# Kernel tuning notes

Measured on AMD Instinct MI355X. Metric: run time of the kernel, lower is better.

## Reference

```python
import jax, jax.numpy as jnp
import numpy as np

DIM = 1024
N_HEADS = 16
HEAD_DIM = DIM // N_HEADS
SCALE = HEAD_DIM ** -0.5


def setup_inputs() -> dict:
    key = jax.random.key(0)
    kx, kq, kk, kv = jax.random.split(key, 4)
    x = jax.random.normal(kx, (2, 2048, DIM), dtype=jnp.float32)
    bv_q = jax.random.normal(kq, (N_HEADS, HEAD_DIM), dtype=jnp.float32) * 0.02
    bv_k = jax.random.normal(kk, (N_HEADS, HEAD_DIM), dtype=jnp.float32) * 0.02
    bv_v = jax.random.normal(kv, (N_HEADS, HEAD_DIM), dtype=jnp.float32) * 0.02
    return {"x": x, "bv_q": bv_q, "bv_k": bv_k, "bv_v": bv_v}


def reference(x, bv_q, bv_k, bv_v):
    B, T, D = x.shape
    H, HD = N_HEADS, HEAD_DIM
    x_h = x.reshape(B, T, H, HD)
    # sign-gated Q/K/V (sign of binding vectors; elementwise +/-1 gating)
    Q = x_h * jnp.sign(bv_q)  # [B,T,H,HD]
    K = x_h * jnp.sign(bv_k)
    V = x_h * jnp.sign(bv_v)
    # causal scores, sigmoid gating (no softmax)
    scores = jnp.einsum('bqhd,bkhd->bhqk', Q, K) * SCALE  # [B,H,T,T]
    causal = jnp.tril(jnp.ones((T, T), dtype=bool))
    attn = jnp.where(causal, jax.nn.sigmoid(scores * 4.0), 0.0)
    out = jnp.einsum('bhqk,bkhd->bqhd', attn, V)  # [B,T,H,HD]
    return out.reshape(B, T, D)
```

## Files before the change

kernel.cpp:

```cpp
#include <hip/hip_runtime.h>
#include <hip/hip_bf16.h>
#include <stdint.h>

#define DIM 1024
#define T_LEN 2048
#define NB 2
#define NH 16
#define HD 64
#define NQT 32

typedef float f32x2 __attribute__((ext_vector_type(2)));
typedef float f32x4 __attribute__((ext_vector_type(4)));
typedef float f32x16 __attribute__((ext_vector_type(16)));
typedef __bf16 bf16x8 __attribute__((ext_vector_type(8)));
typedef __bf16 bf16x2 __attribute__((ext_vector_type(2)));
typedef unsigned int u32;
typedef unsigned int u32x4 __attribute__((ext_vector_type(4)));

#define TK(qt, lo, cnt, dst) ((u32)((qt) | ((lo) << 6) | ((cnt) << 12) | ((dst) << 18)))
__constant__ u32 TASKS[80] = {
    TK(31,0,16,1), TK(31,16,16,2), TK(30,15,16,2), TK(15,0,16,0),
    TK(30,0,15,1), TK(29,0,15,1),  TK(29,15,15,2), TK(28,14,15,2), TK(14,0,15,0),
    TK(28,0,14,1), TK(27,0,14,1),  TK(27,14,14,2), TK(26,13,14,2), TK(13,0,14,0),
    TK(26,0,13,1), TK(25,0,13,1),  TK(25,13,13,2), TK(24,12,13,2), TK(12,0,13,0),
    TK(24,0,12,1), TK(23,0,12,1),  TK(23,12,12,2), TK(22,11,12,2), TK(11,0,12,0),
    TK(22,0,11,1), TK(21,0,11,1),  TK(21,11,11,2), TK(20,10,11,2), TK(10,0,11,0),
    TK(20,0,10,1), TK(19,0,10,1),  TK(19,10,10,2), TK(18,9,10,2),  TK(9,0,10,0),
    TK(18,0,9,1),  TK(17,0,9,1),   TK(17,9,9,2),   TK(16,8,9,2),   TK(8,0,9,0),
    TK(16,0,8,1),  TK(7,0,8,0),
    TK(6,0,7,0), TK(5,0,6,0), TK(4,0,5,0), TK(3,0,4,0),
    TK(2,0,3,0), TK(1,0,2,0), TK(0,0,1,0),
    TK(31,0,32,0), TK(30,0,31,0), TK(29,0,30,0), TK(28,0,29,0),
    TK(27,0,28,0), TK(26,0,27,0), TK(25,0,26,0), TK(24,0,25,0),
    TK(23,0,24,0), TK(22,0,23,0), TK(21,0,22,0), TK(20,0,21,0),
    TK(19,0,20,0), TK(18,0,19,0), TK(17,0,18,0), TK(16,0,17,0),
    TK(15,0,16,0), TK(14,0,15,0), TK(13,0,14,0), TK(12,0,13,0),
    TK(11,0,12,0), TK(10,0,11,0), TK(9,0,10,0),  TK(8,0,9,0),
    TK(7,0,8,0),   TK(6,0,7,0),   TK(5,0,6,0),   TK(4,0,5,0),
    TK(3,0,4,0),   TK(2,0,3,0),   TK(1,0,2,0),   TK(0,0,1,0),
};
#define NSPLIT 48

__device__ __forceinline__ float sgnf(float v) {
    return (v > 0.f) ? 1.f : ((v < 0.f) ? -1.f : 0.f);
}

__device__ __forceinline__ float sigmoid_half(float v) {
    return __builtin_amdgcn_rcpf(1.f + __builtin_amdgcn_exp2f(-0.72134752f * v));
}

__device__ __forceinline__ u32 pack2(float p0, float p1) {
    bf16x2 t = {(__bf16)p0, (__bf16)p1};
    return __builtin_bit_cast(u32, t);
}

__device__ __forceinline__ void gload16(const __bf16* g, __bf16* l) {
    __builtin_amdgcn_global_load_lds(
        (__attribute__((address_space(1))) void*)g,
        (__attribute__((address_space(3))) void*)l,
        16, 0, 0);
}

__global__ __launch_bounds__(256) void prep_kernel(
    const float* __restrict__ x, const float* __restrict__ bvv,
    __bf16* __restrict__ xb, __bf16* __restrict__ xt)
{
    __shared__ __align__(16) __bf16 tile[64][72];

    const int bid = blockIdx.x;
    const int h = bid & 15, tmp = bid >> 4, tt = tmp & 31, b = tmp >> 5;
    const int tid = threadIdx.x;
    const int r = tid >> 2, c0 = (tid & 3) * 16;

    const size_t rowbase = ((size_t)(b * T_LEN + tt * 64 + r)) * DIM + h * HD + c0;
    const float* xp = x + rowbase;

    __bf16 v[16];
    #pragma unroll
    for (int i = 0; i < 16; i += 4) {
        f32x4 f = *(const f32x4*)(xp + i);
        #pragma unroll
        for (int j = 0; j < 4; ++j) v[i + j] = (__bf16)f[j];
    }
    bf16x8 s0, s1;
    #pragma unroll
    for (int j = 0; j < 8; ++j) { s0[j] = v[j]; s1[j] = v[8 + j]; }
    *(bf16x8*)(xb + rowbase)     = s0;
    *(bf16x8*)(xb + rowbase + 8) = s1;
    *(bf16x8*)&tile[r][c0]     = s0;
    *(bf16x8*)&tile[r][c0 + 8] = s1;

    __syncthreads();

    const int d = tid >> 2, t0c = (tid & 3) * 16;
    const float g = sgnf(bvv[h * HD + d]);
    __bf16 ov[16];
    #pragma unroll
    for (int i = 0; i < 16; ++i) ov[i] = (__bf16)((float)tile[t0c + i][d] * g);
    bf16x8 o0, o1;
    #pragma unroll
    for (int j = 0; j < 8; ++j) { o0[j] = ov[j]; o1[j] = ov[8 + j]; }
    const size_t obase = ((size_t)((b * NH + h) * HD + d)) * T_LEN + tt * 64 + t0c;
    *(bf16x8*)(xt + obase)     = o0;
    *(bf16x8*)(xt + obase + 8) = o1;
}

__global__ __launch_bounds__(256, 4) void mba_main(
    const __bf16* __restrict__ xb, const __bf16* __restrict__ xt,
    const float* __restrict__ bvq, const float* __restrict__ bvk,
    float* __restrict__ out, float* __restrict__ ws2, int tbase)
{
    __shared__ __align__(16) __bf16 Kb[3][64][64];
    __shared__ __align__(16) __bf16 Vb[2][64][64];

    const int bid = blockIdx.x;
    const u32 tk = TASKS[tbase + (bid >> 5)];
    const int qt  = tk & 63;
    const int lo  = (tk >> 6) & 63;
    const int CL  = (tk >> 12) & 63;
    const int dst = tk >> 18;

    const int bh = bid & 31;
    const int b = bh >> 4, h = bh & 15;
    const int q0 = qt * 64;

    const int tid = threadIdx.x;
    const int w = tid >> 6, l = tid & 63;
    const int c = l & 31, hi = l >> 5;
    const int qh = w & 1, sh = w >> 1;

    const size_t xb_bh = (size_t)b * T_LEN * DIM + h * HD;
    const size_t xt_bh = (size_t)((b * NH + h) * HD) * T_LEN;

    const int rr = l >> 3;
    const int sw = ((l & 7) ^ rr) << 3;

    auto STAGE_K = [&](int buf, int kvt) {
        const int kv0s = kvt * 64;
        #pragma unroll
        for (int pt = 0; pt < 2; ++pt) {
            const int r0 = w * 8 + pt * 32;
            gload16(xb + xb_bh + (size_t)(kv0s + r0 + rr) * DIM + sw, &Kb[buf][r0][0]);
        }
    };
    auto STAGE_V = [&](int buf, int kvt) {
        const int kv0s = kvt * 64;
        #pragma unroll
        for (int pt = 0; pt < 2; ++pt) {
            const int r0 = w * 8 + pt * 32;
            gload16(xt + xt_bh + (size_t)(r0 + rr) * T_LEN + kv0s + sw, &Vb[buf][r0][0]);
        }
    };

    STAGE_K(0, lo);
    STAGE_V(0, lo);
    if (CL >= 2) STAGE_K(1, lo + 1);

    bf16x8 qa[4];
    {
        const float* bq = bvq + h * HD;
        const float* bk = bvk + h * HD;
        const int qrow = q0 + qh * 32 + c;
        #pragma unroll
        for (int m = 0; m < 4; ++m) {
            const int d0 = m * 16 + hi * 8;
            bf16x8 va = *(const bf16x8*)(xb + xb_bh + (size_t)qrow * DIM + d0);
            #pragma unroll
            for (int j = 0; j < 8; ++j) {
                float f = sgnf(bq[d0 + j]) * sgnf(bk[d0 + j]);
                qa[m][j] = (__bf16)((float)va[j] * f);
            }
        }
    }

    f32x16 o[2];
    #pragma unroll
    for (int nd = 0; nd < 2; ++nd)
        #pragma unroll
        for (int i = 0; i < 16; ++i) o[nd][i] = 0.f;

    int cur = 0;
    const int krow = sh * 32 + c;
    const int swz = (c & 7) << 4;

    for (int lt = 0; lt < CL; ++lt) {
        const int gt = lo + lt;
        const bool last_local = (lt == CL - 1);
        const bool diag = (gt == qt);
        if (last_local) { asm volatile("s_waitcnt vmcnt(0)" ::: "memory"); }
        else            { asm volatile("s_waitcnt vmcnt(2)" ::: "memory"); }
        __builtin_amdgcn_sched_barrier(0);
        __builtin_amdgcn_s_barrier();
        __builtin_amdgcn_sched_barrier(0);

        if (lt + 1 < CL) STAGE_V((lt + 1) & 1, gt + 1);
        __builtin_amdgcn_sched_barrier(0);
        if (lt + 2 < CL) {
            int stg = cur + 2; if (stg >= 3) stg -= 3;
            STAGE_K(stg, gt + 2);
        }
        __builtin_amdgcn_sched_barrier(0);

        f32x16 ss;
        #pragma unroll
        for (int i = 0; i < 16; ++i) ss[i] = 0.f;
        #pragma unroll
        for (int m = 0; m < 4; ++m) {
            bf16x8 kf = *(const bf16x8*)((const char*)&Kb[cur][krow][0]
                          + ((m * 32 + hi * 16) ^ swz));
            ss = __builtin_amdgcn_mfma_f32_32x32x16_bf16(kf, qa[m], ss, 0, 0, 0);
        }

        u32 W[8];
        #pragma unroll
        for (int i = 0; i < 8; ++i) {
            const int r0 = 2 * i;
            const int sl = (r0 & 3) + 8 * (r0 >> 2) + 4 * hi;
            float p0 = sigmoid_half(ss[r0]);
            float p1 = sigmoid_half(ss[r0 + 1]);
            if (diag) {
                const int sg = sh * 32 + sl;
                const int qg = qh * 32 + c;
                if (sg > qg)     p0 = 0.f;
                if (sg + 1 > qg) p1 = 0.f;
            }
            W[i] = pack2(p0, p1);
        }

        asm volatile("v_permlane32_swap_b32 %0, %1" : "+v"(W[0]), "+v"(W[2]));
        asm volatile("v_permlane32_swap_b32 %0, %1" : "+v"(W[1]), "+v"(W[3]));
        asm volatile("v_permlane32_swap_b32 %0, %1" : "+v"(W[4]), "+v"(W[6]));
        asm volatile("v_permlane32_swap_b32 %0, %1" : "+v"(W[5]), "+v"(W[7]));
        bf16x8 pa[2];
        pa[0] = __builtin_bit_cast(bf16x8, (u32x4){W[0], W[1], W[2], W[3]});
        pa[1] = __builtin_bit_cast(bf16x8, (u32x4){W[4], W[5], W[6], W[7]});

        #pragma unroll
        for (int m = 0; m < 2; ++m) {
            #pragma unroll
            for (int nd = 0; nd < 2; ++nd) {
                bf16x8 vf = *(const bf16x8*)((const char*)&Vb[lt & 1][nd * 32 + c][0]
                              + ((sh * 64 + m * 32 + hi * 16) ^ swz));
                o[nd] = __builtin_amdgcn_mfma_f32_32x32x16_bf16(pa[m], vf, o[nd], 0, 0, 0);
            }
        }
        cur = (cur == 2) ? 0 : cur + 1;
    }

    __syncthreads();
    float (*osc)[64] = (float(*)[64]) & Kb[0][0][0];

    if (sh == 1) {
        #pragma unroll
        for (int r = 0; r < 16; ++r) {
            const int qloc = (r & 3) + 8 * (r >> 2) + 4 * hi;
            osc[qh * 32 + qloc][c]      = o[0][r];
            osc[qh * 32 + qloc][32 + c] = o[1][r];
        }
    }
    __syncthreads();
    if (sh == 0) {
        if (dst == 0) {
            #pragma unroll
            for (int r = 0; r < 16; ++r) {
                const int qloc = (r & 3) + 8 * (r >> 2) + 4 * hi;
                const size_t row = (size_t)(b * T_LEN + q0 + qh * 32 + qloc) * DIM + h * HD;
                out[row + c]      = o[0][r] + osc[qh * 32 + qloc][c];
                out[row + 32 + c] = o[1][r] + osc[qh * 32 + qloc][32 + c];
            }
        } else {
            float* wp = ws2 + (size_t)((((qt - 16) * 32 + bh) * 2) + (dst - 1)) * 4096;
            #pragma unroll
            for (int r = 0; r < 16; ++r) {
                const int qloc = (r & 3) + 8 * (r >> 2) + 4 * hi;
                const int qrow = qh * 32 + qloc;
                wp[qrow * 64 + c]      = o[0][r] + osc[qrow][c];
                wp[qrow * 64 + 32 + c] = o[1][r] + osc[qrow][32 + c];
            }
        }
    }
}

__global__ __launch_bounds__(256) void reduce_kernel(
    const float* __restrict__ ws2, float* __restrict__ out)
{
    const int bid = blockIdx.x;
    const int tile = bid >> 2, q4 = bid & 3;
    const int qtw = tile >> 5, bh = tile & 31;
    const int b = bh >> 4, h = bh & 15;

    const float* pa = ws2 + (size_t)((qtw * 32 + bh) * 2) * 4096;
    const float* pb = pa + 4096;

    const int e = q4 * 1024 + threadIdx.x * 4;
    const int qr = e >> 6, d = e & 63;

    f32x4 va = *(const f32x4*)(pa + e);
    f32x4 vb = *(const f32x4*)(pb + e);
    f32x4 s = va + vb;
    *(f32x4*)(out + (size_t)(b * T_LEN + (16 + qtw) * 64 + qr) * DIM + h * HD + d) = s;
}

__global__ __launch_bounds__(256) void mba_fallback(
    const float* __restrict__ x,
    const float* __restrict__ bvq,
    const float* __restrict__ bvk,
    const float* __restrict__ bvv,
    float* __restrict__ out)
{
    __shared__ __align__(16) __bf16 Kb[64][72];
    __shared__ __align__(16) __bf16 Vt[HD][72];
    __shared__ __align__(16) __bf16 Pb[4][16][72];

    const int bid = blockIdx.x;
    const int qt  = (NQT - 1) - (bid & (NQT - 1));
    const int bh  = bid >> 5;
    const int b   = bh >> 4;
    const int h   = bh & 15;

    const int tid = threadIdx.x;
    const int w   = tid >> 6;
    const int l   = tid & 63;
    const int lq  = l & 15;
    const int lh  = l >> 4;

    const int  q0    = qt * 64;
    const long xbase = ((long)b * T_LEN) * DIM + h * HD;

    bf16x8 qa[2];
    {
        const int   qrow = q0 + w * 16 + lq;
        const float* qp  = x + xbase + (long)qrow * DIM + lh * 8;
        const float* gp  = bvq + h * HD + lh * 8;
        #pragma unroll
        for (int ks = 0; ks < 2; ++ks)
            #pragma unroll
            for (int j = 0; j < 8; ++j)
                qa[ks][j] = (__bf16)(qp[ks * 32 + j] * sgnf(gp[ks * 32 + j]));
    }

    f32x4 o[4];
    #pragma unroll
    for (int n = 0; n < 4; ++n) o[n] = (f32x4){0.f, 0.f, 0.f, 0.f};

    const int r_st = tid >> 2;
    const int c0   = (tid & 3) * 16;
    const float* gk = bvk + h * HD + c0;
    const float* gv = bvv + h * HD + c0;

    for (int kvt = 0; kvt <= qt; ++kvt) {
        const int kv0 = kvt * 64;
        __syncthreads();
        {
            const float* kp = x + xbase + (long)(kv0 + r_st) * DIM + c0;
            __bf16 kb[16];
            #pragma unroll
            for (int i = 0; i < 16; ++i) kb[i] = (__bf16)(kp[i] * sgnf(gk[i]));
            *(bf16x8*)&Kb[r_st][c0]     = *(bf16x8*)&kb[0];
            *(bf16x8*)&Kb[r_st][c0 + 8] = *(bf16x8*)&kb[8];
            #pragma unroll
            for (int i = 0; i < 16; ++i)
                Vt[c0 + i][r_st] = (__bf16)(kp[i] * sgnf(gv[i]));
        }
        __syncthreads();

        f32x4 s[4];
        #pragma unroll
        for (int n = 0; n < 4; ++n) s[n] = (f32x4){0.f, 0.f, 0.f, 0.f};
        #pragma unroll
        for (int ks = 0; ks < 2; ++ks)
            #pragma unroll
            for (int n = 0; n < 4; ++n) {
                bf16x8 kf = *(const bf16x8*)&Kb[n * 16 + lq][ks * 32 + lh * 8];
                s[n] = __builtin_amdgcn_mfma_f32_16x16x32_bf16(qa[ks], kf, s[n], 0, 0, 0);
            }

        const bool diag = (kvt == qt);
        #pragma unroll
        for (int n = 0; n < 4; ++n)
            #pragma unroll
            for (int j = 0; j < 4; ++j) {
                float sc = s[n][j];
                float p = __builtin_amdgcn_rcpf(
                              1.f + __builtin_amdgcn_exp2f(-0.72134752f * sc));
                if (diag && (n * 16 + lq) > (w * 16 + lh * 4 + j)) p = 0.f;
                Pb[w][lh * 4 + j][n * 16 + lq] = (__bf16)p;
            }

        #pragma unroll
        for (int ks = 0; ks < 2; ++ks) {
            bf16x8 pf = *(const bf16x8*)&Pb[w][lq][ks * 32 + lh * 8];
            #pragma unroll
            for (int n = 0; n < 4; ++n) {
                bf16x8 vf = *(const bf16x8*)&Vt[n * 16 + lq][ks * 32 + lh * 8];
                o[n] = __builtin_amdgcn_mfma_f32_16x16x32_bf16(pf, vf, o[n], 0, 0, 0);
            }
        }
    }

    float* op = out + ((long)b * T_LEN + q0 + w * 16) * DIM + h * HD;
    #pragma unroll
    for (int n = 0; n < 4; ++n)
        #pragma unroll
        for (int j = 0; j < 4; ++j)
            op[(long)(lh * 4 + j) * DIM + n * 16 + lq] = o[n][j];
}

extern "C" void kernel_launch(void* const* d_in, const int* in_sizes, int n_in,
                              void* d_out, int out_size, void* d_ws, size_t ws_size,
                              hipStream_t stream) {
    (void)in_sizes; (void)n_in; (void)out_size;
    const float* x   = (const float*)d_in[0];
    const float* bvq = (const float*)d_in[1];
    const float* bvk = (const float*)d_in[2];
    const float* bvv = (const float*)d_in[3];
    float* out = (float*)d_out;

    const size_t XB_BYTES = (size_t)NB * T_LEN * DIM * sizeof(__bf16);
    const size_t XT_BYTES = XB_BYTES;
    const size_t W2_BYTES = (size_t)16 * 32 * 2 * 4096 * sizeof(float);

    if (ws_size < XB_BYTES + XT_BYTES) {
        mba_fallback<<<NB * NH * NQT, 256, 0, stream>>>(x, bvq, bvk, bvv, out);
        return;
    }

    __bf16* xb = (__bf16*)d_ws;
    __bf16* xt = xb + (size_t)NB * T_LEN * DIM;

    prep_kernel<<<NB * NQT * NH, 256, 0, stream>>>(x, bvv, xb, xt);

    if (ws_size >= XB_BYTES + XT_BYTES + W2_BYTES) {
        float* ws2 = (float*)((char*)d_ws + XB_BYTES + XT_BYTES);
        mba_main<<<NSPLIT * 32, 256, 0, stream>>>(xb, xt, bvq, bvk, out, ws2, 0);
        reduce_kernel<<<2048, 256, 0, stream>>>(ws2, out);
    } else {
        mba_main<<<32 * 32, 256, 0, stream>>>(xb, xt, bvq, bvk, out, nullptr, 48);
    }
}
```

Before: 53.63 us.

## Precompute gated Q in prep, unroll KV loop by six with static buffer indices

The prep kernel now also writes a Q tensor pre-multiplied by sign(bq)*sign(bk), so the main kernel loads Q fragments directly instead of recomputing the gating per element. The main loop is unrolled by six with compile-time K (triple) and V (double) buffer indices, and the staging addresses advance through pointer increments. The sigmoid uses a packed multiply/add form and a v_cvt_pk_bf16_f32 instruction. The cost is an extra 8MB workspace write and read, plus larger code.

```diff
diff --git a/kernel.cpp b/kernel.cpp
--- a/kernel.cpp
+++ b/kernel.cpp
@@ -16,6 +16,8 @@
 typedef __bf16 bf16x2 __attribute__((ext_vector_type(2)));
 typedef unsigned int u32;
 typedef unsigned int u32x4 __attribute__((ext_vector_type(4)));
+
+template <int N> struct ICT { static constexpr int v = N; };
 
 #define TK(qt, lo, cnt, dst) ((u32)((qt) | ((lo) << 6) | ((cnt) << 12) | ((dst) << 18)))
 __constant__ u32 TASKS[80] = {
@@ -45,15 +47,6 @@
     return (v > 0.f) ? 1.f : ((v < 0.f) ? -1.f : 0.f);
 }
 
-__device__ __forceinline__ float sigmoid_half(float v) {
-    return __builtin_amdgcn_rcpf(1.f + __builtin_amdgcn_exp2f(-0.72134752f * v));
-}
-
-__device__ __forceinline__ u32 pack2(float p0, float p1) {
-    bf16x2 t = {(__bf16)p0, (__bf16)p1};
-    return __builtin_bit_cast(u32, t);
-}
-
 __device__ __forceinline__ void gload16(const __bf16* g, __bf16* l) {
     __builtin_amdgcn_global_load_lds(
         (__attribute__((address_space(1))) void*)g,
@@ -62,8 +55,9 @@
 }
 
 __global__ __launch_bounds__(256) void prep_kernel(
-    const float* __restrict__ x, const float* __restrict__ bvv,
-    __bf16* __restrict__ xb, __bf16* __restrict__ xt)
+    const float* __restrict__ x, const float* __restrict__ bvq,
+    const float* __restrict__ bvk, const float* __restrict__ bvv,
+    __bf16* __restrict__ xb, __bf16* __restrict__ xq, __bf16* __restrict__ xt)
 {
     __shared__ __align__(16) __bf16 tile[64][72];
 
@@ -75,18 +69,27 @@
     const size_t rowbase = ((size_t)(b * T_LEN + tt * 64 + r)) * DIM + h * HD + c0;
     const float* xp = x + rowbase;
 
-    __bf16 v[16];
+    float f[16];
     #pragma unroll
     for (int i = 0; i < 16; i += 4) {
-        f32x4 f = *(const f32x4*)(xp + i);
-        #pragma unroll
-        for (int j = 0; j < 4; ++j) v[i + j] = (__bf16)f[j];
-    }
-    bf16x8 s0, s1;
-    #pragma unroll
-    for (int j = 0; j < 8; ++j) { s0[j] = v[j]; s1[j] = v[8 + j]; }
+        f32x4 v4 = *(const f32x4*)(xp + i);
+        #pragma unroll
+        for (int j = 0; j < 4; ++j) f[i + j] = v4[j];
+    }
+    bf16x8 s0, s1, g0, g1;
+    #pragma unroll
+    for (int j = 0; j < 8; ++j) {
+        s0[j] = (__bf16)f[j];
+        s1[j] = (__bf16)f[8 + j];
+        float gq0 = sgnf(bvq[h * HD + c0 + j])     * sgnf(bvk[h * HD + c0 + j]);
+        float gq1 = sgnf(bvq[h * HD + c0 + 8 + j]) * sgnf(bvk[h * HD + c0 + 8 + j]);
+        g0[j] = (__bf16)(f[j] * gq0);
+        g1[j] = (__bf16)(f[8 + j] * gq1);
+    }
     *(bf16x8*)(xb + rowbase)     = s0;
     *(bf16x8*)(xb + rowbase + 8) = s1;
+    *(bf16x8*)(xq + rowbase)     = g0;
+    *(bf16x8*)(xq + rowbase + 8) = g1;
     *(bf16x8*)&tile[r][c0]     = s0;
     *(bf16x8*)&tile[r][c0 + 8] = s1;
 
@@ -106,8 +109,8 @@
 }
 
 __global__ __launch_bounds__(256, 4) void mba_main(
-    const __bf16* __restrict__ xb, const __bf16* __restrict__ xt,
-    const float* __restrict__ bvq, const float* __restrict__ bvk,
+    const __bf16* __restrict__ xq, const __bf16* __restrict__ xb,
+    const __bf16* __restrict__ xt,
     float* __restrict__ out, float* __restrict__ ws2, int tbase)
 {
     __shared__ __align__(16) __bf16 Kb[3][64][64];
@@ -135,42 +138,29 @@
     const int rr = l >> 3;
     const int sw = ((l & 7) ^ rr) << 3;
 
-    auto STAGE_K = [&](int buf, int kvt) {
-        const int kv0s = kvt * 64;
-        #pragma unroll
-        for (int pt = 0; pt < 2; ++pt) {
-            const int r0 = w * 8 + pt * 32;
-            gload16(xb + xb_bh + (size_t)(kv0s + r0 + rr) * DIM + sw, &Kb[buf][r0][0]);
-        }
-    };
-    auto STAGE_V = [&](int buf, int kvt) {
-        const int kv0s = kvt * 64;
-        #pragma unroll
-        for (int pt = 0; pt < 2; ++pt) {
-            const int r0 = w * 8 + pt * 32;
-            gload16(xt + xt_bh + (size_t)(r0 + rr) * T_LEN + kv0s + sw, &Vb[buf][r0][0]);
-        }
-    };
-
-    STAGE_K(0, lo);
-    STAGE_V(0, lo);
-    if (CL >= 2) STAGE_K(1, lo + 1);
+    const __bf16* kst = xb + xb_bh + (size_t)(lo * 64 + w * 8 + rr) * DIM + sw;
+    const __bf16* vst = xt + xt_bh + (size_t)(w * 8 + rr) * T_LEN + lo * 64 + sw;
+    const size_t KROW32 = (size_t)32 * DIM;
+    const size_t VROW32 = (size_t)32 * T_LEN;
+    const size_t KTILE  = (size_t)64 * DIM;
+
+    gload16(kst,          &Kb[0][w * 8][0]);
+    gload16(kst + KROW32, &Kb[0][w * 8 + 32][0]);
+    gload16(vst,          &Vb[0][w * 8][0]);
+    gload16(vst + VROW32, &Vb[0][w * 8 + 32][0]);
+    if (CL >= 2) {
+        gload16(kst + KTILE,          &Kb[1][w * 8][0]);
+        gload16(kst + KTILE + KROW32, &Kb[1][w * 8 + 32][0]);
+    }
+    kst += 2 * KTILE;
+    vst += 64;
 
     bf16x8 qa[4];
     {
-        const float* bq = bvq + h * HD;
-        const float* bk = bvk + h * HD;
-        const int qrow = q0 + qh * 32 + c;
-        #pragma unroll
-        for (int m = 0; m < 4; ++m) {
-            const int d0 = m * 16 + hi * 8;
-            bf16x8 va = *(const bf16x8*)(xb + xb_bh + (size_t)qrow * DIM + d0);
-            #pragma unroll
-            for (int j = 0; j < 8; ++j) {
-                float f = sgnf(bq[d0 + j]) * sgnf(bk[d0 + j]);
-                qa[m][j] = (__bf16)((float)va[j] * f);
-            }
-        }
+        const __bf16* qp = xq + xb_bh + (size_t)(q0 + qh * 32 + c) * DIM + hi * 8;
+        #pragma unroll
+        for (int m = 0; m < 4; ++m)
+            qa[m] = *(const bf16x8*)(qp + m * 16);
     }
 
     f32x16 o[2];
@@ -179,25 +169,30 @@
         #pragma unroll
         for (int i = 0; i < 16; ++i) o[nd][i] = 0.f;
 
-    int cur = 0;
     const int krow = sh * 32 + c;
     const int swz = (c & 7) << 4;
 
-    for (int lt = 0; lt < CL; ++lt) {
-        const int gt = lo + lt;
-        const bool last_local = (lt == CL - 1);
-        const bool diag = (gt == qt);
-        if (last_local) { asm volatile("s_waitcnt vmcnt(0)" ::: "memory"); }
-        else            { asm volatile("s_waitcnt vmcnt(2)" ::: "memory"); }
+    auto body = [&](int lt, auto kbT, auto vbT) {
+        constexpr int KB = decltype(kbT)::v;
+        constexpr int VB = decltype(vbT)::v;
+        const bool last = (lt == CL - 1);
+        const bool diag = (lo + lt == qt);
+        if (last) { asm volatile("s_waitcnt vmcnt(0)" ::: "memory"); }
+        else      { asm volatile("s_waitcnt vmcnt(2)" ::: "memory"); }
         __builtin_amdgcn_sched_barrier(0);
         __builtin_amdgcn_s_barrier();
         __builtin_amdgcn_sched_barrier(0);
 
-        if (lt + 1 < CL) STAGE_V((lt + 1) & 1, gt + 1);
+        if (lt + 1 < CL) {
+            gload16(vst,          &Vb[VB ^ 1][w * 8][0]);
+            gload16(vst + VROW32, &Vb[VB ^ 1][w * 8 + 32][0]);
+            vst += 64;
+        }
         __builtin_amdgcn_sched_barrier(0);
         if (lt + 2 < CL) {
-            int stg = cur + 2; if (stg >= 3) stg -= 3;
-            STAGE_K(stg, gt + 2);
+            gload16(kst,          &Kb[(KB + 2) % 3][w * 8][0]);
+            gload16(kst + KROW32, &Kb[(KB + 2) % 3][w * 8 + 32][0]);
+            kst += KTILE;
         }
         __builtin_amdgcn_sched_barrier(0);
 
@@ -206,7 +201,7 @@
         for (int i = 0; i < 16; ++i) ss[i] = 0.f;
         #pragma unroll
         for (int m = 0; m < 4; ++m) {
-            bf16x8 kf = *(const bf16x8*)((const char*)&Kb[cur][krow][0]
+            bf16x8 kf = *(const bf16x8*)((const char*)&Kb[KB][krow][0]
                           + ((m * 32 + hi * 16) ^ swz));
             ss = __builtin_amdgcn_mfma_f32_32x32x16_bf16(kf, qa[m], ss, 0, 0, 0);
         }
@@ -215,36 +210,50 @@
         #pragma unroll
         for (int i = 0; i < 8; ++i) {
             const int r0 = 2 * i;
-            const int sl = (r0 & 3) + 8 * (r0 >> 2) + 4 * hi;
-            float p0 = sigmoid_half(ss[r0]);
-            float p1 = sigmoid_half(ss[r0 + 1]);
+            f32x2 z; z.x = ss[r0]; z.y = ss[r0 + 1];
+            z = z * (-0.72134752f);
+            f32x2 e;
+            e.x = __builtin_amdgcn_exp2f(z.x);
+            e.y = __builtin_amdgcn_exp2f(z.y);
+            e = e + 1.0f;
+            float p0 = __builtin_amdgcn_rcpf(e.x);
+            float p1 = __builtin_amdgcn_rcpf(e.y);
             if (diag) {
+                const int sl = (r0 & 3) + 8 * (r0 >> 2) + 4 * hi;
                 const int sg = sh * 32 + sl;
                 const int qg = qh * 32 + c;
                 if (sg > qg)     p0 = 0.f;
                 if (sg + 1 > qg) p1 = 0.f;
             }
-            W[i] = pack2(p0, p1);
+            asm("v_cvt_pk_bf16_f32 %0, %1, %2" : "=v"(W[i]) : "v"(p0), "v"(p1));
         }
 
         asm volatile("v_permlane32_swap_b32 %0, %1" : "+v"(W[0]), "+v"(W[2]));
         asm volatile("v_permlane32_swap_b32 %0, %1" : "+v"(W[1]), "+v"(W[3]));
         asm volatile("v_permlane32_swap_b32 %0, %1" : "+v"(W[4]), "+v"(W[6]));
         asm volatile("v_permlane32_swap_b32 %0, %1" : "+v"(W[5]), "+v"(W[7]));
-        bf16x8 pa[2];
-        pa[0] = __builtin_bit_cast(bf16x8, (u32x4){W[0], W[1], W[2], W[3]});
-        pa[1] = __builtin_bit_cast(bf16x8, (u32x4){W[4], W[5], W[6], W[7]});
+        bf16x8 pa0 = __builtin_bit_cast(bf16x8, (u32x4){W[0], W[1], W[2], W[3]});
+        bf16x8 pa1 = __builtin_bit_cast(bf16x8, (u32x4){W[4], W[5], W[6], W[7]});
 
         #pragma unroll
         for (int m = 0; m < 2; ++m) {
+            const bf16x8 paM = m ? pa1 : pa0;
             #pragma unroll
             for (int nd = 0; nd < 2; ++nd) {
-                bf16x8 vf = *(const bf16x8*)((const char*)&Vb[lt & 1][nd * 32 + c][0]
+                bf16x8 vf = *(const bf16x8*)((const char*)&Vb[VB][nd * 32 + c][0]
                               + ((sh * 64 + m * 32 + hi * 16) ^ swz));
-                o[nd] = __builtin_amdgcn_mfma_f32_32x32x16_bf16(pa[m], vf, o[nd], 0, 0, 0);
-            }
-        }
-        cur = (cur == 2) ? 0 : cur + 1;
+                o[nd] = __builtin_amdgcn_mfma_f32_32x32x16_bf16(paM, vf, o[nd], 0, 0, 0);
+            }
+        }
+    };
+
+    for (int t = 0; t < CL; t += 6) {
+        body(t, ICT<0>{}, ICT<0>{});
+        if (t + 1 < CL) body(t + 1, ICT<1>{}, ICT<1>{});
+        if (t + 2 < CL) body(t + 2, ICT<2>{}, ICT<0>{});
+        if (t + 3 < CL) body(t + 3, ICT<0>{}, ICT<1>{});
+        if (t + 4 < CL) body(t + 4, ICT<1>{}, ICT<0>{});
+        if (t + 5 < CL) body(t + 5, ICT<2>{}, ICT<1>{});
     }
 
     __syncthreads();
@@ -417,24 +426,26 @@
     float* out = (float*)d_out;
 
     const size_t XB_BYTES = (size_t)NB * T_LEN * DIM * sizeof(__bf16);
+    const size_t XQ_BYTES = XB_BYTES;
     const size_t XT_BYTES = XB_BYTES;
     const size_t W2_BYTES = (size_t)16 * 32 * 2 * 4096 * sizeof(float);
 
-    if (ws_size < XB_BYTES + XT_BYTES) {
+    if (ws_size < XB_BYTES + XQ_BYTES + XT_BYTES) {
         mba_fallback<<<NB * NH * NQT, 256, 0, stream>>>(x, bvq, bvk, bvv, out);
         return;
     }
 
     __bf16* xb = (__bf16*)d_ws;
-    __bf16* xt = xb + (size_t)NB * T_LEN * DIM;
-
-    prep_kernel<<<NB * NQT * NH, 256, 0, stream>>>(x, bvv, xb, xt);
-
-    if (ws_size >= XB_BYTES + XT_BYTES + W2_BYTES) {
-        float* ws2 = (float*)((char*)d_ws + XB_BYTES + XT_BYTES);
-        mba_main<<<NSPLIT * 32, 256, 0, stream>>>(xb, xt, bvq, bvk, out, ws2, 0);
+    __bf16* xq = xb + (size_t)NB * T_LEN * DIM;
+    __bf16* xt = xq + (size_t)NB * T_LEN * DIM;
+
+    prep_kernel<<<NB * NQT * NH, 256, 0, stream>>>(x, bvq, bvk, bvv, xb, xq, xt);
+
+    if (ws_size >= XB_BYTES + XQ_BYTES + XT_BYTES + W2_BYTES) {
+        float* ws2 = (float*)((char*)d_ws + XB_BYTES + XQ_BYTES + XT_BYTES);
+        mba_main<<<NSPLIT * 32, 256, 0, stream>>>(xq, xb, xt, out, ws2, 0);
         reduce_kernel<<<2048, 256, 0, stream>>>(ws2, out);
     } else {
-        mba_main<<<32 * 32, 256, 0, stream>>>(xb, xt, bvq, bvk, out, nullptr, 48);
-    }
-}
+        mba_main<<<32 * 32, 256, 0, stream>>>(xq, xb, xt, out, nullptr, 48);
+    }
+}
```

After: 50.46 us. -5.9%, faster.
